# Performance work log

Measured on AMD Instinct MI355X. Metric: run time of the kernel, lower is better.

Reference implementation:

```python
import jax, jax.numpy as jnp
import numpy as np

N_NODES = 100000
N_EDGES = 1600000
C = 64          # in = hidden = out channels
L = 3           # num_layers
BN_EPS = 1e-5


def setup_inputs() -> dict:
    key = jax.random.key(0)
    ks = jax.random.split(key, 16)
    x = jax.random.normal(ks[0], (N_NODES, C), dtype=jnp.float32)
    edge_index = jax.random.randint(ks[1], (2, N_EDGES), 0, N_NODES, dtype=jnp.int32)
    s = 1.0 / np.sqrt(C)
    # Stacked per-layer parameters (all layers are C->C).
    # Linear weights stored as [in, out] (i.e. torch weight transposed).
    W1 = jax.random.normal(ks[2], (L, C, C), dtype=jnp.float32) * s
    b1 = jnp.zeros((L, C), dtype=jnp.float32)
    g1 = jnp.ones((L, C), dtype=jnp.float32)    # MLP BN1 gamma
    be1 = jnp.zeros((L, C), dtype=jnp.float32)  # MLP BN1 beta
    W2 = jax.random.normal(ks[3], (L, C, C), dtype=jnp.float32) * s
    b2 = jnp.zeros((L, C), dtype=jnp.float32)
    g2 = jnp.ones((L, C), dtype=jnp.float32)
    be2 = jnp.zeros((L, C), dtype=jnp.float32)
    bn_g = jnp.ones((L, C), dtype=jnp.float32)   # outer per-layer BN gamma
    bn_be = jnp.zeros((L, C), dtype=jnp.float32)
    eps = jnp.zeros((L,), dtype=jnp.float32)     # GIN eps per layer
    return {"x": x, "edge_index": edge_index, "eps": eps,
            "W1": W1, "b1": b1, "g1": g1, "be1": be1,
            "W2": W2, "b2": b2, "g2": g2, "be2": be2,
            "bn_g": bn_g, "bn_be": bn_be}


def _bn(h, g, b):
    # Inference-mode BatchNorm1d with running_mean=0, running_var=1.
    return g * (h * (1.0 / np.sqrt(1.0 + BN_EPS))) + b


def reference(x, edge_index, eps, W1, b1, g1, be1, W2, b2, g2, be2, bn_g, bn_be):
    src, dst = edge_index[0], edge_index[1]
    for i in range(L):
        # GIN message passing: gather source features, scatter-add to targets.
        agg = jax.ops.segment_sum(x[src], dst, num_segments=N_NODES)  # [N, C]
        h = (1.0 + eps[i]) * x + agg
        # 2-layer MLP: Linear -> BN -> ReLU, twice.
        h = jax.nn.relu(_bn(h @ W1[i] + b1[i], g1[i], be1[i]))
        h = jax.nn.relu(_bn(h @ W2[i] + b2[i], g2[i], be2[i]))
        # Outer per-layer BatchNorm.
        x = _bn(h, bn_g[i], bn_be[i])
        if i < L - 1:
            x = jax.nn.relu(x)  # dropout is identity in eval mode
    return x
```

## Files before the change

### kernel.cpp

```cpp
#include <hip/hip_runtime.h>
#include <hip/hip_fp16.h>

#define N_NODES 100000
#define N_EDGES 1600000
#define CH 64
#define NLAYERS 3
#define NBUCKC 98
#define SLABC 18432
#define NFINE (NBUCKC*8)
#define SLABF 2560
#define EPB 4096

typedef _Float16 half8 __attribute__((ext_vector_type(8)));
typedef float floatx4 __attribute__((ext_vector_type(4)));

static __device__ __forceinline__ float4 ld4(const float* p){ return *(const float4*)p; }
static __device__ __forceinline__ unsigned pack2(float a, float b){
  __half2 h = __float22half2_rn(make_float2(a, b));
  return *(unsigned*)&h;
}
static __device__ __forceinline__ half8 ldh8(const unsigned short* p){
  uint4 u = *(const uint4*)p;
  return *(half8*)&u;
}

__global__ __launch_bounds__(256) void part1_kernel(const int* __restrict__ src, const int* __restrict__ dst,
                                                    int* __restrict__ btail, int* __restrict__ pairs){
  __shared__ int lpos[NBUCKC];
  __shared__ int gb[NBUCKC];
  int tid = threadIdx.x;
  if (tid < NBUCKC) lpos[tid] = 0;
  __syncthreads();
  int base = blockIdx.x * EPB;
  int es[EPB/256], ed[EPB/256], er[EPB/256];
  #pragma unroll
  for (int k = 0; k < EPB/256; ++k) {
    int e = base + k*256 + tid;
    if (e < N_EDGES) {
      es[k] = src[e];
      ed[k] = dst[e];
      er[k] = atomicAdd(&lpos[ed[k] >> 10], 1);
    }
  }
  __syncthreads();
  if (tid < NBUCKC) {
    int cc = lpos[tid];
    gb[tid] = cc ? atomicAdd(&btail[tid], cc) : 0;
  }
  __syncthreads();
  #pragma unroll
  for (int k = 0; k < EPB/256; ++k) {
    int e = base + k*256 + tid;
    if (e < N_EDGES) {
      int bk = ed[k] >> 10;
      int idx = gb[bk] + er[k];
      if (idx < (bk+1)*SLABC)
        pairs[idx] = es[k] | ((ed[k] & 1023) << 20);
    }
  }
}

__global__ __launch_bounds__(256) void csrf_kernel(const int* __restrict__ pairs, const int* __restrict__ btail,
                                                   int* __restrict__ offs, int* __restrict__ offe,
                                                   int* __restrict__ srclist){
  __shared__ int q[SLABF];
  __shared__ int qn;
  __shared__ int c[128];
  __shared__ int s[128];
  __shared__ int cur[128];
  int t = threadIdx.x;
  int f = blockIdx.x;
  int b = f >> 3;
  unsigned sub = f & 7;
  if (t == 0) qn = 0;
  if (t < 128) c[t] = 0;
  __syncthreads();
  int e0c = b*SLABC;
  int e1c = btail[b]; int emax = e0c + SLABC; if (e1c > emax) e1c = emax;
  int lane = t & 63;
  for (int ib = e0c; ib < e1c; ib += 256) {
    int i = ib + t;
    bool valid = (i < e1c);
    int p = valid ? pairs[i] : 0;
    bool m = valid && (((unsigned)p >> 27) == sub);
    unsigned long long mask = __ballot(m);
    if (mask) {
      int leader = __ffsll((long long)mask) - 1;
      int cnt = __popcll(mask);
      int basep = 0;
      if (lane == leader) basep = atomicAdd(&qn, cnt);
      basep = __shfl(basep, leader, 64);
      if (m) {
        int rank = __popcll(mask & ((1ull << lane) - 1ull));
        int pos = basep + rank;
        if (pos < SLABF)
          q[pos] = p;
        atomicAdd(&c[((unsigned)p >> 20) & 127], 1);
      }
    }
  }
  __syncthreads();
  int v = (t < 128) ? c[t] : 0;
  if (t < 128) s[t] = v;
  __syncthreads();
  #pragma unroll
  for (int o = 1; o < 128; o <<= 1){
    int u = 0;
    if (t < 128 && t >= o) u = s[t-o];
    __syncthreads();
    if (t < 128) s[t] += u;
    __syncthreads();
  }
  int e0 = f*SLABF;
  if (t < 128) {
    int excl = s[t] - v;
    cur[t] = excl;
    int n = (f >> 3)*1024 + (f & 7)*128 + t;
    if (n < N_NODES) { offs[n] = e0 + excl; offe[n] = e0 + excl + v; }
  }
  __syncthreads();
  int qn2 = qn; if (qn2 > SLABF) qn2 = SLABF;
  for (int i = t; i < qn2; i += 256) {
    int p = q[i];
    int pos = atomicAdd(&cur[((unsigned)p >> 20) & 127], 1);
    if (pos < SLABF)
      srclist[e0 + pos] = p & 0xFFFFF;
  }
}

__global__ __launch_bounds__(256) void prep_kernel(
    const float* __restrict__ W1, const float* __restrict__ b1,
    const float* __restrict__ g1, const float* __restrict__ be1,
    const float* __restrict__ W2, const float* __restrict__ b2,
    const float* __restrict__ g2, const float* __restrict__ be2,
    const float* __restrict__ bng, const float* __restrict__ bnb,
    _Float16* __restrict__ Wt, float* __restrict__ bf, float* __restrict__ ogb,
    int* __restrict__ btail){
  const float s = 0.9999950000374997f;
  int i = blockIdx.x*256 + threadIdx.x;
  if (i < NBUCKC) btail[i] = i*SLABC;
  if (i < NLAYERS*4096) {
    int l = i >> 12, rem = i & 4095, k = rem >> 6, n = rem & 63;
    int di = n*64 + (((k>>3) ^ (n&7))<<3) + (k&7);
    Wt[l*8192 + di]        = (_Float16)(W1[i] * g1[l*64+n] * s);
    Wt[l*8192 + 4096 + di] = (_Float16)(W2[i] * g2[l*64+n] * s);
  }
  if (i < NLAYERS*64) {
    int l = i >> 6, j = i & 63;
    bf[l*128 + j]      = b1[i]*g1[i]*s + be1[i];
    bf[l*128 + 64 + j] = b2[i]*g2[i]*s + be2[i];
    ogb[i]                 = bng[i]*s;
    ogb[NLAYERS*64 + i]    = bnb[i];
  }
}

__global__ __launch_bounds__(256) void xcvt_kernel(const float* __restrict__ x, unsigned short* __restrict__ xb){
  int i = (blockIdx.x*256 + threadIdx.x)*8;
  if (i < N_NODES*CH) {
    float4 v0 = ld4(x + i), v1 = ld4(x + i + 4);
    uint4 w;
    w.x = pack2(v0.x, v0.y); w.y = pack2(v0.z, v0.w);
    w.z = pack2(v1.x, v1.y); w.w = pack2(v1.z, v1.w);
    *(uint4*)(xb + i) = w;
  }
}

__global__ __launch_bounds__(256, 8) void layer_kernel(const unsigned short* __restrict__ XBin,
                                                    const int* __restrict__ offs, const int* __restrict__ offe,
                                                    const int* __restrict__ srclist,
                                                    const float* __restrict__ eps,
                                                    const _Float16* __restrict__ Wt,
                                                    const float* __restrict__ bf, const float* __restrict__ ogb,
                                                    int layer, float* __restrict__ outf,
                                                    _Float16* __restrict__ outb, int relu_out){
  __shared__ _Float16 HsA[64*64];
  __shared__ _Float16 Wts[64*64];
  int tid = threadIdx.x;
  int b = blockIdx.x;
  const _Float16* Wg = Wt + layer*8192;
  *(uint4*)&Wts[tid*8]       = *(const uint4*)&Wg[tid*8];
  *(uint4*)&Wts[(tid+256)*8] = *(const uint4*)&Wg[(tid+256)*8];

  float ep = 1.0f + eps[layer];
  int kb = tid & 7;
  const unsigned short* xr = XBin + (kb << 3);
  #pragma unroll
  for (int p = 0; p < 2; ++p) {
    int nl = p*32 + (tid >> 3);
    int n = b*64 + nl;
    float r[8] = {0,0,0,0,0,0,0,0};
    if (n < N_NODES) {
      half8 A = (half8)(_Float16)0, B = A, C = A, D = A, E = A, F = A, G = A, H = A;
      int e0 = offs[n], e1 = offe[n];
      int e = e0;
      if (e + 8 <= e1) {
        half8 u0 = ldh8(xr + (srclist[e  ]<<6));
        half8 u1 = ldh8(xr + (srclist[e+1]<<6));
        half8 u2 = ldh8(xr + (srclist[e+2]<<6));
        half8 u3 = ldh8(xr + (srclist[e+3]<<6));
        half8 u4 = ldh8(xr + (srclist[e+4]<<6));
        half8 u5 = ldh8(xr + (srclist[e+5]<<6));
        half8 u6 = ldh8(xr + (srclist[e+6]<<6));
        half8 u7 = ldh8(xr + (srclist[e+7]<<6));
        e += 8;
        for (; e + 8 <= e1; e += 8) {
          half8 v0 = ldh8(xr + (srclist[e  ]<<6));
          half8 v1 = ldh8(xr + (srclist[e+1]<<6));
          half8 v2 = ldh8(xr + (srclist[e+2]<<6));
          half8 v3 = ldh8(xr + (srclist[e+3]<<6));
          half8 v4 = ldh8(xr + (srclist[e+4]<<6));
          half8 v5 = ldh8(xr + (srclist[e+5]<<6));
          half8 v6 = ldh8(xr + (srclist[e+6]<<6));
          half8 v7 = ldh8(xr + (srclist[e+7]<<6));
          A += u0; B += u1; C += u2; D += u3;
          E += u4; F += u5; G += u6; H += u7;
          u0 = v0; u1 = v1; u2 = v2; u3 = v3;
          u4 = v4; u5 = v5; u6 = v6; u7 = v7;
        }
        A += u0; B += u1; C += u2; D += u3;
        E += u4; F += u5; G += u6; H += u7;
      }
      for (; e+4 <= e1; e += 4) {
        half8 u0 = ldh8(xr + (srclist[e  ]<<6));
        half8 u1 = ldh8(xr + (srclist[e+1]<<6));
        half8 u2 = ldh8(xr + (srclist[e+2]<<6));
        half8 u3 = ldh8(xr + (srclist[e+3]<<6));
        A += u0; B += u1; C += u2; D += u3;
      }
      for (; e < e1; ++e) {
        A += ldh8(xr + (srclist[e]<<6));
      }
      half8 S = ((A + B) + (C + D)) + ((E + F) + (G + H));
      half8 sv = ldh8(xr + (n<<6));
      #pragma unroll
      for (int i = 0; i < 8; ++i) r[i] = fmaf(ep, (float)sv[i], (float)S[i]);
    }
    uint4 w;
    w.x = pack2(r[0], r[1]); w.y = pack2(r[2], r[3]);
    w.z = pack2(r[4], r[5]); w.w = pack2(r[6], r[7]);
    *(uint4*)&HsA[nl*64 + ((kb ^ (nl&7))<<3)] = w;
  }
  __syncthreads();

  int lane = tid & 63;
  int wid = tid >> 6;
  int c = lane & 15;
  int q = lane >> 4;
  int mbase = wid*16;
  int ma = mbase + c;

  half8 a0 = *(const half8*)&HsA[ma*64 + (((q)   ^ (ma&7))<<3)];
  half8 a1 = *(const half8*)&HsA[ma*64 + (((4+q) ^ (ma&7))<<3)];

  floatx4 acc[4];
  #pragma unroll
  for (int nt = 0; nt < 4; ++nt) {
    int n = nt*16 + c;
    float bv = bf[layer*128 + n];
    floatx4 Acc = {bv, bv, bv, bv};
    half8 b0 = *(const half8*)&Wts[n*64 + (((q)   ^ (n&7))<<3)];
    half8 b1 = *(const half8*)&Wts[n*64 + (((4+q) ^ (n&7))<<3)];
    Acc = __builtin_amdgcn_mfma_f32_16x16x32_f16(a0, b0, Acc, 0, 0, 0);
    Acc = __builtin_amdgcn_mfma_f32_16x16x32_f16(a1, b1, Acc, 0, 0, 0);
    acc[nt] = Acc;
  }
  __syncthreads();

  #pragma unroll
  for (int nt = 0; nt < 4; ++nt) {
    int n = nt*16 + c;
    #pragma unroll
    for (int r = 0; r < 4; ++r) {
      int m = mbase + q*4 + r;
      float h = acc[nt][r]; h = h > 0.f ? h : 0.f;
      HsA[m*64 + (((n>>3) ^ (m&7))<<3) + (n&7)] = (_Float16)h;
    }
  }
  *(uint4*)&Wts[tid*8]       = *(const uint4*)&Wg[4096 + tid*8];
  *(uint4*)&Wts[(tid+256)*8] = *(const uint4*)&Wg[4096 + (tid+256)*8];
  __syncthreads();

  half8 c0 = *(const half8*)&HsA[ma*64 + (((q)   ^ (ma&7))<<3)];
  half8 c1 = *(const half8*)&HsA[ma*64 + (((4+q) ^ (ma&7))<<3)];
  floatx4 acc2[4];
  #pragma unroll
  for (int nt = 0; nt < 4; ++nt) {
    int n = nt*16 + c;
    float bv = bf[layer*128 + 64 + n];
    floatx4 Acc = {bv, bv, bv, bv};
    half8 b0 = *(const half8*)&Wts[n*64 + (((q)   ^ (n&7))<<3)];
    half8 b1 = *(const half8*)&Wts[n*64 + (((4+q) ^ (n&7))<<3)];
    Acc = __builtin_amdgcn_mfma_f32_16x16x32_f16(c0, b0, Acc, 0, 0, 0);
    Acc = __builtin_amdgcn_mfma_f32_16x16x32_f16(c1, b1, Acc, 0, 0, 0);
    acc2[nt] = Acc;
  }

  #pragma unroll
  for (int nt = 0; nt < 4; ++nt) {
    int n = nt*16 + c;
    float og = ogb[layer*64 + n];
    float ob = ogb[NLAYERS*64 + layer*64 + n];
    #pragma unroll
    for (int r = 0; r < 4; ++r) {
      int m = mbase + q*4 + r;
      int gnode = b*64 + m;
      if (gnode < N_NODES) {
        float h = acc2[nt][r]; h = h > 0.f ? h : 0.f;
        float o = fmaf(og, h, ob);
        if (relu_out) {
          o = o > 0.f ? o : 0.f;
          outb[(size_t)gnode*CH + n] = (_Float16)o;
        } else {
          outf[(size_t)gnode*CH + n] = o;
        }
      }
    }
  }
}

extern "C" void kernel_launch(void* const* d_in, const int* in_sizes, int n_in,
                              void* d_out, int out_size, void* d_ws, size_t ws_size,
                              hipStream_t stream) {
  const float* x0  = (const float*)d_in[0];
  const int*   ei  = (const int*)d_in[1];
  const float* eps = (const float*)d_in[2];
  const float* W1  = (const float*)d_in[3];
  const float* b1  = (const float*)d_in[4];
  const float* g1  = (const float*)d_in[5];
  const float* be1 = (const float*)d_in[6];
  const float* W2  = (const float*)d_in[7];
  const float* b2  = (const float*)d_in[8];
  const float* g2  = (const float*)d_in[9];
  const float* be2 = (const float*)d_in[10];
  const float* bng = (const float*)d_in[11];
  const float* bnb = (const float*)d_in[12];
  const int* src = ei;
  const int* dst = ei + N_EDGES;
  float* OUT = (float*)d_out;

  char* p = (char*)d_ws;
  auto carve = [&](size_t bytes)->char*{ char* r = p; p += (bytes + 255) & ~(size_t)255; return r; };
  int*   offs    = (int*)carve((size_t)N_NODES*sizeof(int));
  int*   offe    = (int*)carve((size_t)N_NODES*sizeof(int));
  int*   btail   = (int*)carve(NBUCKC*sizeof(int));
  int*   pairs   = (int*)carve((size_t)NBUCKC*SLABC*sizeof(int));
  int*   srclist = (int*)carve((size_t)NFINE*SLABF*sizeof(int));
  unsigned short* XB0 = (unsigned short*)carve((size_t)N_NODES*CH*2);
  unsigned short* XB1 = (unsigned short*)carve((size_t)N_NODES*CH*2);
  _Float16* Wt   = (_Float16*)carve((size_t)NLAYERS*2*4096*2);
  float* bfb     = (float*)carve((size_t)NLAYERS*2*64*sizeof(float));
  float* ogb     = (float*)carve((size_t)2*NLAYERS*64*sizeof(float));

  const int npart = (N_EDGES + EPB - 1)/EPB;
  prep_kernel<<<48, 256, 0, stream>>>(W1,b1,g1,be1,W2,b2,g2,be2,bng,bnb,Wt,bfb,ogb,btail);
  part1_kernel<<<npart, 256, 0, stream>>>(src, dst, btail, pairs);
  csrf_kernel<<<NFINE, 256, 0, stream>>>(pairs, btail, offs, offe, srclist);
  xcvt_kernel<<<(N_NODES*CH/8 + 255)/256, 256, 0, stream>>>(x0, XB0);

  const int nlb = (N_NODES + 63)/64;
  layer_kernel<<<nlb, 256, 0, stream>>>(XB0, offs, offe, srclist, eps, Wt, bfb, ogb, 0, OUT, (_Float16*)XB1, 1);
  layer_kernel<<<nlb, 256, 0, stream>>>(XB1, offs, offe, srclist, eps, Wt, bfb, ogb, 1, OUT, (_Float16*)XB0, 1);
  layer_kernel<<<nlb, 256, 0, stream>>>(XB0, offs, offe, srclist, eps, Wt, bfb, ogb, 2, OUT, (_Float16*)XB1, 0);
}
```

Before: 277.1 us.

## Partition edges directly into fine buckets and fuse x conversion into partition

Replaces the two-level bucketing (coarse 1024-node buckets, then each fine block rescanning a whole coarse slab with ballot filtering) with a single partition pass straight into 784 fine 128-node buckets. The CSR kernel then reads only its own fine slab. The separate fp16 conversion kernel of x is folded into the partition kernel as a grid-stride loop, removing one launch. The cost is a larger per-block shared histogram and 200 blocks that each handle 8000 edges with a two-pass read of dst, which lowers parallelism in the partition step.

Result: faster. 271.3 us (-2.1%).

```diff
diff --git a/kernel.cpp b/kernel.cpp
--- a/kernel.cpp
+++ b/kernel.cpp
@@ -5,11 +5,10 @@
 #define N_EDGES 1600000
 #define CH 64
 #define NLAYERS 3
-#define NBUCKC 98
-#define SLABC 18432
-#define NFINE (NBUCKC*8)
+#define NF2 784
 #define SLABF 2560
-#define EPB 4096
+#define NPART 200
+#define EPB2 8000
 
 typedef _Float16 half8 __attribute__((ext_vector_type(8)));
 typedef float floatx4 __attribute__((ext_vector_type(4)));
@@ -24,80 +23,56 @@
   return *(half8*)&u;
 }
 
-__global__ __launch_bounds__(256) void part1_kernel(const int* __restrict__ src, const int* __restrict__ dst,
-                                                    int* __restrict__ btail, int* __restrict__ pairs){
-  __shared__ int lpos[NBUCKC];
-  __shared__ int gb[NBUCKC];
+__global__ __launch_bounds__(256) void part12_kernel(const int* __restrict__ src, const int* __restrict__ dst,
+                                                     int* __restrict__ ftail, int* __restrict__ pairs2,
+                                                     const float* __restrict__ x, unsigned short* __restrict__ xb){
+  __shared__ int hist[NF2];
+  __shared__ int cur[NF2];
   int tid = threadIdx.x;
-  if (tid < NBUCKC) lpos[tid] = 0;
-  __syncthreads();
-  int base = blockIdx.x * EPB;
-  int es[EPB/256], ed[EPB/256], er[EPB/256];
-  #pragma unroll
-  for (int k = 0; k < EPB/256; ++k) {
-    int e = base + k*256 + tid;
-    if (e < N_EDGES) {
-      es[k] = src[e];
-      ed[k] = dst[e];
-      er[k] = atomicAdd(&lpos[ed[k] >> 10], 1);
-    }
-  }
-  __syncthreads();
-  if (tid < NBUCKC) {
-    int cc = lpos[tid];
-    gb[tid] = cc ? atomicAdd(&btail[tid], cc) : 0;
-  }
-  __syncthreads();
-  #pragma unroll
-  for (int k = 0; k < EPB/256; ++k) {
-    int e = base + k*256 + tid;
-    if (e < N_EDGES) {
-      int bk = ed[k] >> 10;
-      int idx = gb[bk] + er[k];
-      if (idx < (bk+1)*SLABC)
-        pairs[idx] = es[k] | ((ed[k] & 1023) << 20);
-    }
-  }
-}
-
-__global__ __launch_bounds__(256) void csrf_kernel(const int* __restrict__ pairs, const int* __restrict__ btail,
-                                                   int* __restrict__ offs, int* __restrict__ offe,
-                                                   int* __restrict__ srclist){
-  __shared__ int q[SLABF];
-  __shared__ int qn;
+  for (int i = tid; i < NF2; i += 256) hist[i] = 0;
+  __syncthreads();
+  int base = blockIdx.x * EPB2;
+  int eend = base + EPB2;
+  for (int e = base + tid; e < eend; e += 256) {
+    atomicAdd(&hist[dst[e] >> 7], 1);
+  }
+  __syncthreads();
+  for (int i = tid; i < NF2; i += 256) {
+    int c = hist[i];
+    cur[i] = c ? atomicAdd(&ftail[i], c) : 0;
+  }
+  __syncthreads();
+  for (int e = base + tid; e < eend; e += 256) {
+    int s = src[e], d = dst[e];
+    int f = d >> 7;
+    int idx = atomicAdd(&cur[f], 1);
+    if (idx < (f+1)*SLABF)
+      pairs2[idx] = s | ((d & 127) << 20);
+  }
+  for (int i = (blockIdx.x*256 + tid)*8; i < N_NODES*CH; i += NPART*256*8) {
+    float4 v0 = ld4(x + i), v1 = ld4(x + i + 4);
+    uint4 w;
+    w.x = pack2(v0.x, v0.y); w.y = pack2(v0.z, v0.w);
+    w.z = pack2(v1.x, v1.y); w.w = pack2(v1.z, v1.w);
+    *(uint4*)(xb + i) = w;
+  }
+}
+
+__global__ __launch_bounds__(256) void csr_kernel(const int* __restrict__ pairs2, const int* __restrict__ ftail,
+                                                  int* __restrict__ offs, int* __restrict__ offe,
+                                                  int* __restrict__ srclist){
   __shared__ int c[128];
   __shared__ int s[128];
   __shared__ int cur[128];
   int t = threadIdx.x;
   int f = blockIdx.x;
-  int b = f >> 3;
-  unsigned sub = f & 7;
-  if (t == 0) qn = 0;
+  int e0 = f*SLABF;
+  int e1 = ftail[f]; int emax = e0 + SLABF; if (e1 > emax) e1 = emax;
   if (t < 128) c[t] = 0;
   __syncthreads();
-  int e0c = b*SLABC;
-  int e1c = btail[b]; int emax = e0c + SLABC; if (e1c > emax) e1c = emax;
-  int lane = t & 63;
-  for (int ib = e0c; ib < e1c; ib += 256) {
-    int i = ib + t;
-    bool valid = (i < e1c);
-    int p = valid ? pairs[i] : 0;
-    bool m = valid && (((unsigned)p >> 27) == sub);
-    unsigned long long mask = __ballot(m);
-    if (mask) {
-      int leader = __ffsll((long long)mask) - 1;
-      int cnt = __popcll(mask);
-      int basep = 0;
-      if (lane == leader) basep = atomicAdd(&qn, cnt);
-      basep = __shfl(basep, leader, 64);
-      if (m) {
-        int rank = __popcll(mask & ((1ull << lane) - 1ull));
-        int pos = basep + rank;
-        if (pos < SLABF)
-          q[pos] = p;
-        atomicAdd(&c[((unsigned)p >> 20) & 127], 1);
-      }
-    }
+  for (int i = e0 + t; i < e1; i += 256) {
+    int p = pairs2[i];
+    atomicAdd(&c[((unsigned)p >> 20) & 127], 1);
   }
   __syncthreads();
   int v = (t < 128) ? c[t] : 0;
@@ -111,17 +86,15 @@
     if (t < 128) s[t] += u;
     __syncthreads();
   }
-  int e0 = f*SLABF;
   if (t < 128) {
     int excl = s[t] - v;
     cur[t] = excl;
-    int n = (f >> 3)*1024 + (f & 7)*128 + t;
+    int n = f*128 + t;
     if (n < N_NODES) { offs[n] = e0 + excl; offe[n] = e0 + excl + v; }
   }
   __syncthreads();
-  int qn2 = qn; if (qn2 > SLABF) qn2 = SLABF;
-  for (int i = t; i < qn2; i += 256) {
-    int p = q[i];
+  for (int i = e0 + t; i < e1; i += 256) {
+    int p = pairs2[i];
     int pos = atomicAdd(&cur[((unsigned)p >> 20) & 127], 1);
     if (pos < SLABF)
       srclist[e0 + pos] = p & 0xFFFFF;
@@ -135,10 +108,10 @@
     const float* __restrict__ g2, const float* __restrict__ be2,
     const float* __restrict__ bng, const float* __restrict__ bnb,
     _Float16* __restrict__ Wt, float* __restrict__ bf, float* __restrict__ ogb,
-    int* __restrict__ btail){
+    int* __restrict__ ftail){
   const float s = 0.9999950000374997f;
   int i = blockIdx.x*256 + threadIdx.x;
-  if (i < NBUCKC) btail[i] = i*SLABC;
+  if (i < NF2) ftail[i] = i*SLABF;
   if (i < NLAYERS*4096) {
     int l = i >> 12, rem = i & 4095, k = rem >> 6, n = rem & 63;
     int di = n*64 + (((k>>3) ^ (n&7))<<3) + (k&7);
@@ -151,17 +124,6 @@
     bf[l*128 + 64 + j] = b2[i]*g2[i]*s + be2[i];
     ogb[i]                 = bng[i]*s;
     ogb[NLAYERS*64 + i]    = bnb[i];
-  }
-}
-
-__global__ __launch_bounds__(256) void xcvt_kernel(const float* __restrict__ x, unsigned short* __restrict__ xb){
-  int i = (blockIdx.x*256 + threadIdx.x)*8;
-  if (i < N_NODES*CH) {
-    float4 v0 = ld4(x + i), v1 = ld4(x + i + 4);
-    uint4 w;
-    w.x = pack2(v0.x, v0.y); w.y = pack2(v0.z, v0.w);
-    w.z = pack2(v1.x, v1.y); w.w = pack2(v1.z, v1.w);
-    *(uint4*)(xb + i) = w;
   }
 }
 
@@ -342,20 +304,18 @@
   auto carve = [&](size_t bytes)->char*{ char* r = p; p += (bytes + 255) & ~(size_t)255; return r; };
   int*   offs    = (int*)carve((size_t)N_NODES*sizeof(int));
   int*   offe    = (int*)carve((size_t)N_NODES*sizeof(int));
-  int*   btail   = (int*)carve(NBUCKC*sizeof(int));
-  int*   pairs   = (int*)carve((size_t)NBUCKC*SLABC*sizeof(int));
-  int*   srclist = (int*)carve((size_t)NFINE*SLABF*sizeof(int));
+  int*   ftail   = (int*)carve(NF2*sizeof(int));
+  int*   pairs2  = (int*)carve((size_t)NF2*SLABF*sizeof(int));
+  int*   srclist = (int*)carve((size_t)NF2*SLABF*sizeof(int));
   unsigned short* XB0 = (unsigned short*)carve((size_t)N_NODES*CH*2);
   unsigned short* XB1 = (unsigned short*)carve((size_t)N_NODES*CH*2);
   _Float16* Wt   = (_Float16*)carve((size_t)NLAYERS*2*4096*2);
   float* bfb     = (float*)carve((size_t)NLAYERS*2*64*sizeof(float));
   float* ogb     = (float*)carve((size_t)2*NLAYERS*64*sizeof(float));
 
-  const int npart = (N_EDGES + EPB - 1)/EPB;
-  prep_kernel<<<48, 256, 0, stream>>>(W1,b1,g1,be1,W2,b2,g2,be2,bng,bnb,Wt,bfb,ogb,btail);
-  part1_kernel<<<npart, 256, 0, stream>>>(src, dst, btail, pairs);
-  csrf_kernel<<<NFINE, 256, 0, stream>>>(pairs, btail, offs, offe, srclist);
-  xcvt_kernel<<<(N_NODES*CH/8 + 255)/256, 256, 0, stream>>>(x0, XB0);
+  prep_kernel<<<48, 256, 0, stream>>>(W1,b1,g1,be1,W2,b2,g2,be2,bng,bnb,Wt,bfb,ogb,ftail);
+  part12_kernel<<<NPART, 256, 0, stream>>>(src, dst, ftail, pairs2, x0, XB0);
+  csr_kernel<<<NF2, 256, 0, stream>>>(pairs2, ftail, offs, offe, srclist);
 
   const int nlb = (N_NODES + 63)/64;
   layer_kernel<<<nlb, 256, 0, stream>>>(XB0, offs, offe, srclist, eps, Wt, bfb, ogb, 0, OUT, (_Float16*)XB1, 1);
```
